# Kernel tuning notes

Hardware: AMD Instinct MI355X
Metric: run time of the kernel (lower is better)

Reference implementation:

```python
import jax, jax.numpy as jnp
import numpy as np
from jax import lax

T = 20            # obs_len + pred_len
S = 256           # number of scenes (segments in seq_start_end)
P = 128           # pedestrians per scene (segments equal-sized for vectorization)
B = S * P         # total pedestrians in batch
MLP = 1024
THR = 0.25        # collision_threshold == minimum_distance
BN_EPS = 1e-5


def setup_inputs() -> dict:
    key = jax.random.key(0)
    k = jax.random.split(key, 8)
    traj = jax.random.uniform(k[0], (T, B, 2), jnp.float32) * 15.0  # positions in meters
    traj_rel = jax.random.normal(k[1], (T, B, 2), jnp.float32)
    starts = jnp.arange(S, dtype=jnp.int32) * P
    seq_start_end = jnp.stack([starts, starts + P], axis=1)  # (S, 2)
    W1 = jax.random.normal(k[2], (1, MLP), jnp.float32)
    b1 = jnp.zeros((MLP,), jnp.float32)
    g1 = jnp.ones((MLP,), jnp.float32)
    beta1 = jnp.zeros((MLP,), jnp.float32)
    W2 = jax.random.normal(k[3], (MLP, 1), jnp.float32) / np.sqrt(MLP)
    b2 = jnp.zeros((1,), jnp.float32)
    g2 = jnp.ones((1,), jnp.float32)
    beta2 = jnp.zeros((1,), jnp.float32)
    return dict(traj=traj, traj_rel=traj_rel, seq_start_end=seq_start_end,
                W1=W1, b1=b1, g1=g1, beta1=beta1, W2=W2, b2=b2, g2=g2, beta2=beta2)


def _batchnorm(x, g, b):
    # nn.BatchNorm1d in train mode: biased batch stats
    mean = jnp.mean(x, axis=0)
    var = jnp.var(x, axis=0)
    return g * (x - mean) * lax.rsqrt(var + BN_EPS) + b


def _collision_rewards(traj):
    # traj: (T, B, 2); segments are equal-sized (P peds per scene) -> reshape
    x = traj.reshape(T, S, P, 2)
    diff = x[:, :, :, None, :] - x[:, :, None, :, :]          # (T,S,P,P,2)
    d = jnp.sqrt(jnp.sum(diff * diff, axis=-1))               # (T,S,P,P) pairwise L2
    d = jnp.where(d == 0.0, THR, d)                           # distance[distance==0]=minimum_distance
    m = jnp.min(jnp.min(d, axis=2), axis=0)                   # min over other peds, then time -> (S,P)
    cols = (m < THR).astype(jnp.float32).reshape(B)           # binary collision indicator
    rewards = (1.0 - cols)[:, None]                           # -1*cols + 1, shape (B,1)
    return lax.stop_gradient(rewards)  # binary threshold: no gradient flows to traj


def reference(traj, traj_rel, seq_start_end, W1, b1, g1, beta1, W2, b2, g2, beta2):
    rewards = _collision_rewards(traj)                        # (B,1)
    h = jax.nn.relu(_batchnorm(rewards @ W1 + b1, g1, beta1)) # Linear->BN->ReLU
    out = jax.nn.relu(_batchnorm(h @ W2 + b2, g2, beta2))     # Linear->BN->ReLU
    return out                                                # (B,1) scores
```

## Files before the change

kernel.cpp:

```cpp
#include <hip/hip_runtime.h>

#define TT 20
#define SS 256
#define PP 128
#define BB (SS * PP)
#define MLPD 1024
#define BN_EPS 1e-5f
#define THR_BITS 0x3D800000u

__global__ __launch_bounds__(512) void collide_kernel(
    const float* __restrict__ traj, unsigned* __restrict__ flags) {
  __shared__ float2 sp[TT * PP];
  __shared__ unsigned red[512];
  const int s = blockIdx.x;
  const int tid = threadIdx.x;

  const float2* g = (const float2*)traj;
  for (int k = tid; k < TT * PP; k += 512) {
    int t = k >> 7;
    int ped = k & 127;
    sp[k] = g[(size_t)t * BB + s * PP + ped];
  }
  __syncthreads();

  const int i = tid & 127;
  const int q = tid >> 7;
  unsigned mn = 0xFFFFFFFFu;
#pragma unroll
  for (int tt = 0; tt < 5; ++tt) {
    const int t = q * 5 + tt;
    const float2 pi = sp[t * PP + i];
    const float xi = pi.x, yi = pi.y;
#pragma unroll 8
    for (int j = 0; j < PP; ++j) {
      float2 pj = sp[t * PP + j];
      float dx = __fsub_rn(xi, pj.x);
      float dy = __fsub_rn(yi, pj.y);
      float d2 = __fadd_rn(__fmul_rn(dx, dx), __fmul_rn(dy, dy));
      unsigned u = __float_as_uint(d2) - 1u;
      mn = (u < mn) ? u : mn;
    }
  }
  red[tid] = mn;
  __syncthreads();
  if (tid < 128) {
    unsigned m0 = red[tid];
    unsigned m1 = red[tid + 128];
    unsigned m2 = red[tid + 256];
    unsigned m3 = red[tid + 384];
    unsigned a = m0 < m1 ? m0 : m1;
    unsigned b = m2 < m3 ? m2 : m3;
    unsigned m = a < b ? a : b;
    flags[s * PP + tid] = (m < (THR_BITS - 1u)) ? 1u : 0u;
  }
}

__global__ __launch_bounds__(1024) void mlp_kernel(
    const unsigned* __restrict__ flags,
    const float* __restrict__ W1, const float* __restrict__ b1,
    const float* __restrict__ g1, const float* __restrict__ beta1,
    const float* __restrict__ W2, const float* __restrict__ b2,
    const float* __restrict__ g2, const float* __restrict__ beta2,
    float* __restrict__ outvals) {
  __shared__ float red0[1024];
  __shared__ float red1[1024];
  __shared__ float sh_p;
  const int tid = threadIdx.x;

  const uint4* f4 = (const uint4*)flags;
  unsigned cnt = 0;
#pragma unroll
  for (int k = 0; k < 8; ++k) {
    uint4 v = f4[tid + k * 1024];
    cnt += v.x + v.y + v.z + v.w;
  }
  red0[tid] = (float)cnt;
  __syncthreads();
  for (int off = 512; off > 0; off >>= 1) {
    if (tid < off) red0[tid] += red0[tid + off];
    __syncthreads();
  }
  if (tid == 0) {
    float ncoll = red0[0];
    sh_p = ((float)BB - ncoll) / (float)BB;
  }
  __syncthreads();
  const float p = sh_p;

  float w = W1[tid], gg = g1[tid], bt = beta1[tid], w2 = W2[tid];
  float rs1 = rsqrtf(p * (1.0f - p) * w * w + BN_EPS);
  float h0 = fmaxf(gg * (-p * w) * rs1 + bt, 0.0f);
  float h1 = fmaxf(gg * ((1.0f - p) * w) * rs1 + bt, 0.0f);
  red0[tid] = h0 * w2;
  red1[tid] = h1 * w2;
  __syncthreads();
  for (int off = 512; off > 0; off >>= 1) {
    if (tid < off) {
      red0[tid] += red0[tid + off];
      red1[tid] += red1[tid + off];
    }
    __syncthreads();
  }
  if (tid == 0) {
    float z0 = red0[0] + b2[0];
    float z1 = red1[0] + b2[0];
    float dz = z1 - z0;
    float rs2 = rsqrtf(p * (1.0f - p) * dz * dz + BN_EPS);
    float o0 = fmaxf(g2[0] * (p * (z0 - z1)) * rs2 + beta2[0], 0.0f);
    float o1 = fmaxf(g2[0] * ((1.0f - p) * dz) * rs2 + beta2[0], 0.0f);
    outvals[0] = o0;
    outvals[1] = o1;
  }
}

__global__ __launch_bounds__(256) void scatter_kernel(
    const unsigned* __restrict__ flags, const float* __restrict__ outvals,
    float* __restrict__ out) {
  int gid = blockIdx.x * 256 + threadIdx.x;
  float o0 = outvals[0];
  float o1 = outvals[1];
  out[gid] = flags[gid] ? o0 : o1;
}

extern "C" void kernel_launch(void* const* d_in, const int* in_sizes, int n_in,
                              void* d_out, int out_size, void* d_ws, size_t ws_size,
                              hipStream_t stream) {
  const float* traj = (const float*)d_in[0];
  const float* W1 = (const float*)d_in[3];
  const float* b1 = (const float*)d_in[4];
  const float* g1 = (const float*)d_in[5];
  const float* beta1 = (const float*)d_in[6];
  const float* W2 = (const float*)d_in[7];
  const float* b2 = (const float*)d_in[8];
  const float* g2 = (const float*)d_in[9];
  const float* beta2 = (const float*)d_in[10];

  unsigned* flags = (unsigned*)d_ws;
  float* outvals = (float*)((char*)d_ws + BB * sizeof(unsigned));
  float* out = (float*)d_out;

  collide_kernel<<<SS, 512, 0, stream>>>(traj, flags);
  mlp_kernel<<<1, 1024, 0, stream>>>(flags, W1, b1, g1, beta1, W2, b2, g2,
                                     beta2, outvals);
  scatter_kernel<<<BB / 256, 256, 0, stream>>>(flags, outvals, out);
}
```

Baseline: 96.89 us.

## Fuse MLP into scatter via per-scene counts and vectorize pairwise distance loop

The collision kernel now reads positions directly from global memory as float4 pairs with packed 2-wide float math instead of staging in shared memory. It also writes a per-scene collision count using wave ballots. The separate single-block MLP kernel and the scatter kernel are merged: every scatter block reduces the 256 counts and recomputes the two output values redundantly, eliminating a serial launch and the 128K-flag reduction. The risks are that uniform global reads in the inner loop may cost more than shared-memory broadcast, and the MLP work is duplicated across blocks.

```diff
diff --git a/kernel.cpp b/kernel.cpp
--- a/kernel.cpp
+++ b/kernel.cpp
@@ -4,41 +4,45 @@
 #define SS 256
 #define PP 128
 #define BB (SS * PP)
-#define MLPD 1024
 #define BN_EPS 1e-5f
 #define THR_BITS 0x3D800000u
 
+typedef float v2f __attribute__((ext_vector_type(2)));
+
 __global__ __launch_bounds__(512) void collide_kernel(
-    const float* __restrict__ traj, unsigned* __restrict__ flags) {
-  __shared__ float2 sp[TT * PP];
+    const float* __restrict__ traj, unsigned* __restrict__ flags,
+    unsigned* __restrict__ counts) {
   __shared__ unsigned red[512];
+  __shared__ unsigned cntpart[2];
   const int s = blockIdx.x;
   const int tid = threadIdx.x;
-
-  const float2* g = (const float2*)traj;
-  for (int k = tid; k < TT * PP; k += 512) {
-    int t = k >> 7;
-    int ped = k & 127;
-    sp[k] = g[(size_t)t * BB + s * PP + ped];
-  }
-  __syncthreads();
-
   const int i = tid & 127;
   const int q = tid >> 7;
+
+  const float2* __restrict__ g2 = (const float2*)traj;
   unsigned mn = 0xFFFFFFFFu;
 #pragma unroll
   for (int tt = 0; tt < 5; ++tt) {
     const int t = q * 5 + tt;
-    const float2 pi = sp[t * PP + i];
-    const float xi = pi.x, yi = pi.y;
+    const float2 pi = g2[(size_t)t * BB + s * PP + i];
+    const v2f piv = {pi.x, pi.y};
+    const float4* __restrict__ row4 =
+        (const float4*)(g2 + (size_t)t * BB + s * PP);
 #pragma unroll 8
-    for (int j = 0; j < PP; ++j) {
-      float2 pj = sp[t * PP + j];
-      float dx = __fsub_rn(xi, pj.x);
-      float dy = __fsub_rn(yi, pj.y);
-      float d2 = __fadd_rn(__fmul_rn(dx, dx), __fmul_rn(dy, dy));
-      unsigned u = __float_as_uint(d2) - 1u;
-      mn = (u < mn) ? u : mn;
+    for (int jj = 0; jj < PP / 2; ++jj) {
+      float4 w = row4[jj];
+      v2f p0 = {w.x, w.y};
+      v2f p1 = {w.z, w.w};
+      v2f d0 = piv - p0;
+      v2f q0 = d0 * d0;
+      float d2a = __fadd_rn(q0.x, q0.y);
+      v2f d1 = piv - p1;
+      v2f q1 = d1 * d1;
+      float d2b = __fadd_rn(q1.x, q1.y);
+      unsigned u0 = __float_as_uint(d2a) - 1u;
+      unsigned u1 = __float_as_uint(d2b) - 1u;
+      unsigned mu = u0 < u1 ? u0 : u1;
+      mn = mu < mn ? mu : mn;
     }
   }
   red[tid] = mn;
@@ -51,75 +55,79 @@
     unsigned a = m0 < m1 ? m0 : m1;
     unsigned b = m2 < m3 ? m2 : m3;
     unsigned m = a < b ? a : b;
-    flags[s * PP + tid] = (m < (THR_BITS - 1u)) ? 1u : 0u;
+    unsigned fl = (m < (THR_BITS - 1u)) ? 1u : 0u;
+    flags[s * PP + tid] = fl;
+    unsigned long long bal = __ballot(fl != 0);
+    if ((tid & 63) == 0) cntpart[tid >> 6] = (unsigned)__popcll(bal);
   }
+  __syncthreads();
+  if (tid == 0) counts[s] = cntpart[0] + cntpart[1];
 }
 
-__global__ __launch_bounds__(1024) void mlp_kernel(
-    const unsigned* __restrict__ flags,
-    const float* __restrict__ W1, const float* __restrict__ b1,
-    const float* __restrict__ g1, const float* __restrict__ beta1,
-    const float* __restrict__ W2, const float* __restrict__ b2,
-    const float* __restrict__ g2, const float* __restrict__ beta2,
-    float* __restrict__ outvals) {
-  __shared__ float red0[1024];
-  __shared__ float red1[1024];
-  __shared__ float sh_p;
+__global__ __launch_bounds__(256) void mlp_scatter_kernel(
+    const unsigned* __restrict__ flags, const unsigned* __restrict__ counts,
+    const float* __restrict__ W1, const float* __restrict__ g1,
+    const float* __restrict__ beta1, const float* __restrict__ W2,
+    const float* __restrict__ g2v, const float* __restrict__ beta2,
+    float* __restrict__ out) {
+  __shared__ float sred0[4];
+  __shared__ float sred1[4];
+  __shared__ float bc[3];
   const int tid = threadIdx.x;
+  const int lane = tid & 63;
+  const int wv = tid >> 6;
 
-  const uint4* f4 = (const uint4*)flags;
-  unsigned cnt = 0;
+  float c = (float)counts[tid];
 #pragma unroll
-  for (int k = 0; k < 8; ++k) {
-    uint4 v = f4[tid + k * 1024];
-    cnt += v.x + v.y + v.z + v.w;
-  }
-  red0[tid] = (float)cnt;
+  for (int o = 32; o > 0; o >>= 1) c += __shfl_down(c, o);
+  if (lane == 0) sred0[wv] = c;
   __syncthreads();
-  for (int off = 512; off > 0; off >>= 1) {
-    if (tid < off) red0[tid] += red0[tid + off];
-    __syncthreads();
-  }
   if (tid == 0) {
-    float ncoll = red0[0];
-    sh_p = ((float)BB - ncoll) / (float)BB;
+    float ncoll = sred0[0] + sred0[1] + sred0[2] + sred0[3];
+    bc[0] = ((float)BB - ncoll) / (float)BB;
   }
   __syncthreads();
-  const float p = sh_p;
+  const float p = bc[0];
+  const float pq = p * (1.0f - p);
 
-  float w = W1[tid], gg = g1[tid], bt = beta1[tid], w2 = W2[tid];
-  float rs1 = rsqrtf(p * (1.0f - p) * w * w + BN_EPS);
-  float h0 = fmaxf(gg * (-p * w) * rs1 + bt, 0.0f);
-  float h1 = fmaxf(gg * ((1.0f - p) * w) * rs1 + bt, 0.0f);
-  red0[tid] = h0 * w2;
-  red1[tid] = h1 * w2;
+  const float4 w = ((const float4*)W1)[tid];
+  const float4 gg = ((const float4*)g1)[tid];
+  const float4 bt = ((const float4*)beta1)[tid];
+  const float4 w2 = ((const float4*)W2)[tid];
+  float s0 = 0.0f, s1 = 0.0f;
+  {
+    const float wv4[4] = {w.x, w.y, w.z, w.w};
+    const float gv4[4] = {gg.x, gg.y, gg.z, gg.w};
+    const float bv4[4] = {bt.x, bt.y, bt.z, bt.w};
+    const float w24[4] = {w2.x, w2.y, w2.z, w2.w};
+#pragma unroll
+    for (int k = 0; k < 4; ++k) {
+      float rs = rsqrtf(pq * wv4[k] * wv4[k] + BN_EPS);
+      float h0 = fmaxf(gv4[k] * (-p * wv4[k]) * rs + bv4[k], 0.0f);
+      float h1 = fmaxf(gv4[k] * ((1.0f - p) * wv4[k]) * rs + bv4[k], 0.0f);
+      s0 += h0 * w24[k];
+      s1 += h1 * w24[k];
+    }
+  }
+#pragma unroll
+  for (int o = 32; o > 0; o >>= 1) {
+    s0 += __shfl_down(s0, o);
+    s1 += __shfl_down(s1, o);
+  }
+  if (lane == 0) { sred0[wv] = s0; sred1[wv] = s1; }
   __syncthreads();
-  for (int off = 512; off > 0; off >>= 1) {
-    if (tid < off) {
-      red0[tid] += red0[tid + off];
-      red1[tid] += red1[tid + off];
-    }
-    __syncthreads();
+  if (tid == 0) {
+    float z0 = sred0[0] + sred0[1] + sred0[2] + sred0[3];
+    float z1 = sred1[0] + sred1[1] + sred1[2] + sred1[3];
+    float dz = z1 - z0;
+    float rs2 = rsqrtf(pq * dz * dz + BN_EPS);
+    bc[1] = fmaxf(g2v[0] * (p * (z0 - z1)) * rs2 + beta2[0], 0.0f);
+    bc[2] = fmaxf(g2v[0] * ((1.0f - p) * dz) * rs2 + beta2[0], 0.0f);
   }
-  if (tid == 0) {
-    float z0 = red0[0] + b2[0];
-    float z1 = red1[0] + b2[0];
-    float dz = z1 - z0;
-    float rs2 = rsqrtf(p * (1.0f - p) * dz * dz + BN_EPS);
-    float o0 = fmaxf(g2[0] * (p * (z0 - z1)) * rs2 + beta2[0], 0.0f);
-    float o1 = fmaxf(g2[0] * ((1.0f - p) * dz) * rs2 + beta2[0], 0.0f);
-    outvals[0] = o0;
-    outvals[1] = o1;
-  }
-}
+  __syncthreads();
 
-__global__ __launch_bounds__(256) void scatter_kernel(
-    const unsigned* __restrict__ flags, const float* __restrict__ outvals,
-    float* __restrict__ out) {
-  int gid = blockIdx.x * 256 + threadIdx.x;
-  float o0 = outvals[0];
-  float o1 = outvals[1];
-  out[gid] = flags[gid] ? o0 : o1;
+  const int gid = blockIdx.x * 256 + tid;
+  out[gid] = flags[gid] ? bc[1] : bc[2];
 }
 
 extern "C" void kernel_launch(void* const* d_in, const int* in_sizes, int n_in,
@@ -127,20 +135,17 @@
                               hipStream_t stream) {
   const float* traj = (const float*)d_in[0];
   const float* W1 = (const float*)d_in[3];
-  const float* b1 = (const float*)d_in[4];
   const float* g1 = (const float*)d_in[5];
   const float* beta1 = (const float*)d_in[6];
   const float* W2 = (const float*)d_in[7];
-  const float* b2 = (const float*)d_in[8];
   const float* g2 = (const float*)d_in[9];
   const float* beta2 = (const float*)d_in[10];
 
   unsigned* flags = (unsigned*)d_ws;
-  float* outvals = (float*)((char*)d_ws + BB * sizeof(unsigned));
+  unsigned* counts = (unsigned*)d_ws + BB;
   float* out = (float*)d_out;
 
-  collide_kernel<<<SS, 512, 0, stream>>>(traj, flags);
-  mlp_kernel<<<1, 1024, 0, stream>>>(flags, W1, b1, g1, beta1, W2, b2, g2,
-                                     beta2, outvals);
-  scatter_kernel<<<BB / 256, 256, 0, stream>>>(flags, outvals, out);
+  collide_kernel<<<SS, 512, 0, stream>>>(traj, flags, counts);
+  mlp_scatter_kernel<<<BB / 256, 256, 0, stream>>>(flags, counts, W1, g1,
+                                                   beta1, W2, g2, beta2, out);
 }
```

Result: no change. 97.00 us (+0.1%).
